# Kernel tuning notes

Measured on AMD Instinct MI355X. Metric: run time of the kernel, lower is better.

Reference implementation:

```python
import jax, jax.numpy as jnp
import numpy as np

B, S, D, H, L, DFF, WIN = 2, 2048, 768, 12, 2, 3072, 512
EPS = 1e-5
DH = D // H


def setup_inputs() -> dict:
    key = jax.random.key(0)
    ks = jax.random.split(key, 8)
    rn = lambda k, shape: jax.random.normal(k, shape, jnp.float32) * 0.02
    inp = {
        "src": jax.random.normal(ks[0], (B, S, D), jnp.float32),
        "qw": rn(ks[1], (L, D, D)), "qb": jnp.zeros((L, D), jnp.float32),
        "kw": rn(ks[2], (L, D, D)), "kb": jnp.zeros((L, D), jnp.float32),
        "vw": rn(ks[3], (L, D, D)), "vb": jnp.zeros((L, D), jnp.float32),
        "ow": rn(ks[4], (L, D, D)), "ob": jnp.zeros((L, D), jnp.float32),
        "w1": rn(ks[5], (L, DFF, D)), "b1": jnp.zeros((L, DFF), jnp.float32),
        "w2": rn(ks[6], (L, D, DFF)), "b2": jnp.zeros((L, D), jnp.float32),
        "g1": jnp.ones((L, D), jnp.float32), "be1": jnp.zeros((L, D), jnp.float32),
        "g2": jnp.ones((L, D), jnp.float32), "be2": jnp.zeros((L, D), jnp.float32),
    }
    return inp


def _ln(x, g, b):
    m = jnp.mean(x, axis=-1, keepdims=True)
    v = jnp.mean(jnp.square(x - m), axis=-1, keepdims=True)
    return (x - m) * jax.lax.rsqrt(v + EPS) * g + b


def _encoder(src, qw, qb, kw, kb, vw, vb, ow, ob, w1, b1, w2, b2, g1, be1, g2, be2):
    scale = DH ** -0.5
    idx = jnp.arange(S)
    # non-causal sliding window: |i - j| <= window_size // 2
    band = jnp.abs(idx[:, None] - idx[None, :]) <= (WIN // 2)
    neg = -jnp.finfo(jnp.float32).max
    x = src
    for l in range(L):
        # projections -> (B, H, S, DH)
        q = (x @ qw[l].T + qb[l]).reshape(B, S, H, DH).transpose(0, 2, 1, 3)
        k = (x @ kw[l].T + kb[l]).reshape(B, S, H, DH).transpose(0, 2, 1, 3)
        v = (x @ vw[l].T + vb[l]).reshape(B, S, H, DH).transpose(0, 2, 1, 3)
        # full dense scores then band mask (faithful to the original module)
        sim = jnp.einsum('bhid,bhjd->bhij', q * scale, k)
        sim = jnp.where(band, sim, neg)
        attn = jax.nn.softmax(sim, axis=-1)
        o = jnp.einsum('bhij,bhjd->bhid', attn, v)
        o = o.transpose(0, 2, 1, 3).reshape(B, S, D) @ ow[l].T + ob[l]
        # post-norm transformer block (norm_first=False)
        x = _ln(x + o, g1[l], be1[l])
        ff = jax.nn.relu(x @ w1[l].T + b1[l]) @ w2[l].T + b2[l]
        x = _ln(x + ff, g2[l], be2[l])
    return x


def reference(src, qw, qb, kw, kb, vw, vb, ow, ob, w1, b1, w2, b2, g1, be1, g2, be2):
    return _encoder(src, qw, qb, kw, kb, vw, vb, ow, ob, w1, b1, w2, b2, g1, be1, g2, be2)
```

## Files before the change

### kernel.cpp

```cpp
#include <hip/hip_runtime.h>
#include <math.h>

#define BATCH 2
#define SEQ   2048
#define DM    768
#define NHD   12
#define NL    2
#define DFF   3072
#define DH    64
#define HW    256
#define MR    (BATCH*SEQ)
#define EPSF  1e-5f
#define SCALE 0.125f
#define QKVS  2304

typedef __attribute__((ext_vector_type(8))) __bf16 bf16x8;
typedef __attribute__((ext_vector_type(4))) float  f32x4;

__device__ __forceinline__ ushort f2bu(float f) {
    union { __bf16 h; ushort u; } c;
    c.h = (__bf16)f;
    return c.u;
}
__device__ __forceinline__ float bu2f(ushort u) {
    union { uint u; float f; } c;
    c.u = ((uint)u) << 16;
    return c.f;
}

__device__ __forceinline__ void gload16(const ushort* g, ushort* l) {
    __builtin_amdgcn_global_load_lds(
        (const __attribute__((address_space(1))) void*)g,
        (__attribute__((address_space(3))) void*)l, 16, 0, 0);
}

__device__ __forceinline__ void xcd_swz(int& bx, int& by, int& bz) {
    const int gx = gridDim.x, gy = gridDim.y;
    const int nwg = gx * gy * gridDim.z;
    int lin = bx + gx * (by + gy * bz);
    lin = (lin & 7) * (nwg >> 3) + (lin >> 3);
    bx = lin % gx;
    int rest = lin / gx;
    by = rest % gy;
    bz = rest / gy;
}

__global__ __launch_bounds__(256) void cvt(const float* __restrict__ in,
                                           ushort* __restrict__ out, int n)
{
    int i = (blockIdx.x * 256 + threadIdx.x) * 4;
    if (i >= n) return;
    float4 v = *(const float4*)(in + i);
    ushort4 o;
    o.x = f2bu(v.x); o.y = f2bu(v.y); o.z = f2bu(v.z); o.w = f2bu(v.w);
    *(ushort4*)(out + i) = o;
}

#define STAGE128(bi, kt) do {                                           \
        const int _k0 = (kt) * 32;                                      \
        gload16(ag + _k0,                    &As[bi][t * 8]);           \
        gload16(ag + (size_t)64 * ldk + _k0, &As[bi][2048 + t * 8]);    \
        gload16(wg + _k0,                    &Ws[bi][t * 8]);           \
        gload16(wg + (size_t)64 * ldk + _k0, &Ws[bi][2048 + t * 8]);    \
    } while (0)

__global__ __launch_bounds__(256) void gemm128(
    const ushort* __restrict__ A, const ushort* __restrict__ W,
    const float* __restrict__ bias, ushort* __restrict__ C,
    float* __restrict__ part, int M, int N, int Kc, int ldk, int relu)
{
    __shared__ ushort As[3][128 * 32];
    __shared__ ushort Ws[3][128 * 32];

    int bxi = blockIdx.x, byi = blockIdx.y, bzi = blockIdx.z;
    xcd_swz(bxi, byi, bzi);

    const int t  = threadIdx.x;
    const int bm = byi * 128;
    const int bn = bxi * 128;
    const int z  = bzi;
    const int kbase = z * Kc;

    const int w    = t >> 6;
    const int lane = t & 63;
    const int quad = lane >> 4;
    const int lrow = lane & 15;
    const int wm   = (w >> 1) * 64;
    const int wn   = (w & 1) * 64;
    const int rx   = (lrow >> 1) & 3;
    const int rq   = (quad ^ rx) * 8;

    const int srow = t >> 2;
    const int scol = (((t & 3) ^ ((t >> 3) & 3)) * 8);
    const ushort* ag = A + (size_t)(bm + srow) * ldk + kbase + scol;
    const ushort* wg = W + (size_t)(bn + srow) * ldk + kbase + scol;

    f32x4 acc[4][4] = {};
    const int NT = Kc / 32;

    STAGE128(0, 0);
    STAGE128(1, 1);

    for (int kt = 0; kt < NT; ++kt) {
        if (kt + 1 < NT)
            asm volatile("s_waitcnt vmcnt(4)" ::: "memory");
        else
            asm volatile("s_waitcnt vmcnt(0)" ::: "memory");
        __builtin_amdgcn_s_barrier();

        const int cb = kt % 3;
        bf16x8 af[4], bfr[4];
#pragma unroll
        for (int i = 0; i < 4; ++i)
            af[i] = *(const bf16x8*)&As[cb][(wm + i * 16 + lrow) * 32 + rq];
#pragma unroll
        for (int j = 0; j < 4; ++j)
            bfr[j] = *(const bf16x8*)&Ws[cb][(wn + j * 16 + lrow) * 32 + rq];

#pragma unroll
        for (int i = 0; i < 4; ++i)
#pragma unroll
            for (int j = 0; j < 4; ++j)
                acc[i][j] = __builtin_amdgcn_mfma_f32_16x16x32_bf16(
                    af[i], bfr[j], acc[i][j], 0, 0, 0);

        if (kt + 2 < NT) {
            const int sb = (kt + 2) % 3;
            STAGE128(sb, kt + 2);
        }
    }

    if (gridDim.z > 1) {
        float* po = part + (size_t)z * M * N;
#pragma unroll
        for (int j = 0; j < 4; ++j) {
            const int col = bn + wn + j * 16 + lrow;
#pragma unroll
            for (int i = 0; i < 4; ++i) {
                const int rb = bm + wm + i * 16 + quad * 4;
#pragma unroll
                for (int r = 0; r < 4; ++r)
                    po[(size_t)(rb + r) * N + col] = acc[i][j][r];
            }
        }
    } else {
#pragma unroll
        for (int j = 0; j < 4; ++j) {
            const int col = bn + wn + j * 16 + lrow;
            const float bv = bias[col];
#pragma unroll
            for (int i = 0; i < 4; ++i) {
                const int rb = bm + wm + i * 16 + quad * 4;
#pragma unroll
                for (int r = 0; r < 4; ++r) {
                    float vv = acc[i][j][r] + bv;
                    if (relu) vv = fmaxf(vv, 0.f);
                    C[(size_t)(rb + r) * N + col] = f2bu(vv);
                }
            }
        }
    }
}

#define STAGE64(bi, kt) do {                                            \
        const int _k0 = (kt) * 32;                                      \
        gload16(ag + _k0,                    &As[bi][t * 8]);           \
        gload16(wg + _k0,                    &Ws[bi][t * 8]);           \
        gload16(wg + (size_t)64 * ldk + _k0, &Ws[bi][2048 + t * 8]);    \
    } while (0)

__global__ __launch_bounds__(256) void gemm64(
    const ushort* __restrict__ A, const ushort* __restrict__ W,
    const float* __restrict__ bias, ushort* __restrict__ C,
    float* __restrict__ part, int M, int N, int Kc, int ldk, int relu)
{
    __shared__ ushort As[3][64 * 32];
    __shared__ ushort Ws[3][128 * 32];

    int bxi = blockIdx.x, byi = blockIdx.y, bzi = blockIdx.z;
    xcd_swz(bxi, byi, bzi);

    const int t  = threadIdx.x;
    const int bm = byi * 64;
    const int bn = bxi * 128;
    const int z  = bzi;
    const int kbase = z * Kc;

    const int w    = t >> 6;
    const int lane = t & 63;
    const int quad = lane >> 4;
    const int lrow = lane & 15;
    const int wm   = (w >> 1) * 32;
    const int wn   = (w & 1) * 64;
    const int rx   = (lrow >> 1) & 3;
    const int rq   = (quad ^ rx) * 8;

    const int srow = t >> 2;
    const int scol = (((t & 3) ^ ((t >> 3) & 3)) * 8);
    const ushort* ag = A + (size_t)(bm + srow) * ldk + kbase + scol;
    const ushort* wg = W + (size_t)(bn + srow) * ldk + kbase + scol;

    f32x4 acc[2][4] = {};
    const int NT = Kc / 32;

    STAGE64(0, 0);
    STAGE64(1, 1);

    for (int kt = 0; kt < NT; ++kt) {
        if (kt + 1 < NT)
            asm volatile("s_waitcnt vmcnt(3)" ::: "memory");
        else
            asm volatile("s_waitcnt vmcnt(0)" ::: "memory");
        __builtin_amdgcn_s_barrier();

        const int cb = kt % 3;
        bf16x8 af[2], bfr[4];
#pragma unroll
        for (int i = 0; i < 2; ++i)
            af[i] = *(const bf16x8*)&As[cb][(wm + i * 16 + lrow) * 32 + rq];
#pragma unroll
        for (int j = 0; j < 4; ++j)
            bfr[j] = *(const bf16x8*)&Ws[cb][(wn + j * 16 + lrow) * 32 + rq];

#pragma unroll
        for (int i = 0; i < 2; ++i)
#pragma unroll
            for (int j = 0; j < 4; ++j)
                acc[i][j] = __builtin_amdgcn_mfma_f32_16x16x32_bf16(
                    af[i], bfr[j], acc[i][j], 0, 0, 0);

        if (kt + 2 < NT) {
            const int sb = (kt + 2) % 3;
            STAGE64(sb, kt + 2);
        }
    }

    if (gridDim.z > 1) {
        float* po = part + (size_t)z * M * N;
#pragma unroll
        for (int j = 0; j < 4; ++j) {
            const int col = bn + wn + j * 16 + lrow;
#pragma unroll
            for (int i = 0; i < 2; ++i) {
                const int rb = bm + wm + i * 16 + quad * 4;
#pragma unroll
                for (int r = 0; r < 4; ++r)
                    po[(size_t)(rb + r) * N + col] = acc[i][j][r];
            }
        }
    } else {
#pragma unroll
        for (int j = 0; j < 4; ++j) {
            const int col = bn + wn + j * 16 + lrow;
            const float bv = bias[col];
#pragma unroll
            for (int i = 0; i < 2; ++i) {
                const int rb = bm + wm + i * 16 + quad * 4;
#pragma unroll
                for (int r = 0; r < 4; ++r) {
                    float vv = acc[i][j][r] + bv;
                    if (relu) vv = fmaxf(vv, 0.f);
                    C[(size_t)(rb + r) * N + col] = f2bu(vv);
                }
            }
        }
    }
}

#define QT  64
#define NCH 9
#define KP  72

__global__ __launch_bounds__(256) void attn(
    const ushort* __restrict__ q, const ushort* __restrict__ k,
    const ushort* __restrict__ v, ushort* __restrict__ o)
{
    __shared__ ushort kv[2][64][KP];
    __shared__ ushort vt[2][64][KP];
    __shared__ ushort sc[QT][KP];

    int bxi = blockIdx.x, byi = blockIdx.y, bzi = blockIdx.z;
    xcd_swz(bxi, byi, bzi);

    const int t    = threadIdx.x;
    const int i0   = bxi * QT;
    const int h    = byi;
    const int b    = bzi;
    const size_t ibase = (size_t)b * SEQ * QKVS + (size_t)h * DH;
    const size_t obase = (size_t)b * SEQ * DM   + (size_t)h * DH;

    const int w    = t >> 6;
    const int lane = t & 63;
    const int quad = lane >> 4;
    const int lrow = lane & 15;
    const int qrow = w * 16;

    const int jstart = i0 - HW;

    const int sjj[2] = { t >> 3, (t + 256) >> 3 };
    const int sd0 = (t & 7) * 8;

#pragma unroll
    for (int e = 0; e < 2; ++e) {
        int idx = t + 256 * e;
        int qi = idx >> 3, d0 = (idx & 7) * 8;
        uint4 raw = *(const uint4*)(q + ibase + (size_t)(i0 + qi) * QKVS + d0);
        *(uint4*)&sc[qi][d0] = raw;
    }
    uint4 kr[2], vr[2];
#pragma unroll
    for (int e = 0; e < 2; ++e) {
        int j = jstart + sjj[e];
        kr[e] = make_uint4(0, 0, 0, 0);
        vr[e] = make_uint4(0, 0, 0, 0);
        if (j >= 0 && j < SEQ) {
            kr[e] = *(const uint4*)(k + ibase + (size_t)j * QKVS + sd0);
            vr[e] = *(const uint4*)(v + ibase + (size_t)j * QKVS + sd0);
        }
    }
#pragma unroll
    for (int e = 0; e < 2; ++e) {
        *(uint4*)&kv[0][sjj[e]][sd0] = kr[e];
        const ushort* u = (const ushort*)&vr[e];
#pragma unroll
        for (int x = 0; x < 8; ++x) {
            int dh  = sd0 + x;
            int blk = ((sjj[e] >> 3) ^ (dh >> 3)) & 7;
            vt[0][dh][blk * 8 + (sjj[e] & 7)] = u[x];
        }
    }
    __syncthreads();

    const bf16x8 a0 = *(const bf16x8*)&sc[qrow + lrow][quad * 8];
    const bf16x8 a1 = *(const bf16x8*)&sc[qrow + lrow][32 + quad * 8];

    float m_s = -1e20f, l_s = 0.f;
    f32x4 oacc[4] = {};

    for (int c = 0; c < NCH; ++c) {
        const int cur = c & 1;
        const int j0  = jstart + c * 64;

        if (c + 1 < NCH) {
            const int j0n = jstart + (c + 1) * 64;
#pragma unroll
            for (int e = 0; e < 2; ++e) {
                int j = j0n + sjj[e];
                kr[e] = make_uint4(0, 0, 0, 0);
                vr[e] = make_uint4(0, 0, 0, 0);
                if (j >= 0 && j < SEQ) {
                    kr[e] = *(const uint4*)(k + ibase + (size_t)j * QKVS + sd0);
                    vr[e] = *(const uint4*)(v + ibase + (size_t)j * QKVS + sd0);
                }
            }
        }

        const bool full = (c >= 1) && (c <= 7) && (j0 >= 0) && (j0 + 64 <= SEQ);
        float p[4][4];
#pragma unroll
        for (int kt = 0; kt < 4; ++kt) {
            const int krow = kt * 16;
            bf16x8 kf0 = *(const bf16x8*)&kv[cur][krow + lrow][quad * 8];
            bf16x8 kf1 = *(const bf16x8*)&kv[cur][krow + lrow][32 + quad * 8];
            f32x4 acc = {};
            acc = __builtin_amdgcn_mfma_f32_16x16x32_bf16(kf0, a0, acc, 0, 0, 0);
            acc = __builtin_amdgcn_mfma_f32_16x16x32_bf16(kf1, a1, acc, 0, 0, 0);
            if (full) {
#pragma unroll
                for (int r = 0; r < 4; ++r) p[kt][r] = acc[r] * SCALE;
            } else {
                const int ig = i0 + qrow + lrow;
#pragma unroll
                for (int r = 0; r < 4; ++r) {
                    const int jg = j0 + krow + quad * 4 + r;
                    bool ok = (jg >= 0) && (jg < SEQ) &&
                              (jg >= ig - HW) && (jg <= ig + HW);
                    p[kt][r] = ok ? acc[r] * SCALE : -1e30f;
                }
            }
        }

        float cm = p[0][0];
#pragma unroll
        for (int kt = 0; kt < 4; ++kt)
#pragma unroll
            for (int r = 0; r < 4; ++r) cm = fmaxf(cm, p[kt][r]);
        cm = fmaxf(cm, __shfl_xor(cm, 16));
        cm = fmaxf(cm, __shfl_xor(cm, 32));

        const bool resc = !__all(cm <= m_s + 8.f);
        float f = 1.f;
        if (resc) {
            const float mn = fmaxf(m_s, cm);
            f = __expf(m_s - mn);
            m_s = mn;
        }
        float cs = 0.f;
#pragma unroll
        for (int kt = 0; kt < 4; ++kt)
#pragma unroll
            for (int r = 0; r < 4; ++r) {
                float e = __expf(p[kt][r] - m_s);
                p[kt][r] = e;
                cs += e;
            }
        cs += __shfl_xor(cs, 16);
        cs += __shfl_xor(cs, 32);
        l_s = l_s * f + cs;
        if (resc) {
            float f4[4];
#pragma unroll
            for (int r = 0; r < 4; ++r) f4[r] = __shfl(f, quad * 4 + r);
#pragma unroll
            for (int nt = 0; nt < 4; ++nt)
#pragma unroll
                for (int r = 0; r < 4; ++r) oacc[nt][r] *= f4[r];
        }

#pragma unroll
        for (int kt = 0; kt < 4; ++kt) {
            ushort4 pw;
            pw.x = f2bu(p[kt][0]);
            pw.y = f2bu(p[kt][1]);
            pw.z = f2bu(p[kt][2]);
            pw.w = f2bu(p[kt][3]);
            *(ushort4*)&sc[qrow + lrow][kt * 16 + quad * 4] = pw;
        }

        bf16x8 pa0 = *(const bf16x8*)&sc[qrow + lrow][quad * 8];
        bf16x8 pa1 = *(const bf16x8*)&sc[qrow + lrow][32 + quad * 8];
#pragma unroll
        for (int nt = 0; nt < 4; ++nt) {
            const int dh  = nt * 16 + lrow;
            const int rsw = (dh >> 3) & 7;
            bf16x8 b0 = *(const bf16x8*)&vt[cur][dh][((quad)     ^ rsw) * 8];
            bf16x8 b1 = *(const bf16x8*)&vt[cur][dh][((quad + 4) ^ rsw) * 8];
            oacc[nt] = __builtin_amdgcn_mfma_f32_16x16x32_bf16(pa0, b0, oacc[nt], 0, 0, 0);
            oacc[nt] = __builtin_amdgcn_mfma_f32_16x16x32_bf16(pa1, b1, oacc[nt], 0, 0, 0);
        }

        if (c + 1 < NCH) {
            const int nxt = cur ^ 1;
#pragma unroll
            for (int e = 0; e < 2; ++e) {
                *(uint4*)&kv[nxt][sjj[e]][sd0] = kr[e];
                const ushort* u = (const ushort*)&vr[e];
#pragma unroll
                for (int x = 0; x < 8; ++x) {
                    int dh  = sd0 + x;
                    int blk = ((sjj[e] >> 3) ^ (dh >> 3)) & 7;
                    vt[nxt][dh][blk * 8 + (sjj[e] & 7)] = u[x];
                }
            }
        }
        __syncthreads();
    }

    const float inv = 1.f / l_s;
    float inv4[4];
#pragma unroll
    for (int r = 0; r < 4; ++r) inv4[r] = __shfl(inv, quad * 4 + r);
#pragma unroll
    for (int r = 0; r < 4; ++r) {
        const int qi = i0 + qrow + quad * 4 + r;
#pragma unroll
        for (int nt = 0; nt < 4; ++nt)
            o[obase + (size_t)qi * DM + nt * 16 + lrow] = f2bu(oacc[nt][r] * inv4[r]);
    }
}

__global__ __launch_bounds__(256) void add_ln_sk(
    const ushort* __restrict__ xa, const float* __restrict__ pp,
    const float* __restrict__ bias, const float* __restrict__ g,
    const float* __restrict__ be,
    ushort* __restrict__ ob, float* __restrict__ of, int fin)
{
    const int r = blockIdx.x * 4 + (threadIdx.x >> 6);
    const int t = threadIdx.x & 63;
    const size_t off = (size_t)r * DM;
    const size_t pl  = (size_t)MR * DM;
    float sv[12];
    float s1 = 0.f, s2 = 0.f;
#pragma unroll
    for (int ii = 0; ii < 12; ++ii) {
        const int c = t + 64 * ii;
        float vv = bu2f(xa[off + c]) + pp[off + c] + pp[pl + off + c] + bias[c];
        sv[ii] = vv; s1 += vv; s2 += vv * vv;
    }
#pragma unroll
    for (int o2 = 32; o2; o2 >>= 1) {
        s1 += __shfl_xor(s1, o2);
        s2 += __shfl_xor(s2, o2);
    }
    const float mean = s1 * (1.f / 768.f);
    const float rstd = rsqrtf(s2 * (1.f / 768.f) - mean * mean + EPSF);
#pragma unroll
    for (int ii = 0; ii < 12; ++ii) {
        const int c = t + 64 * ii;
        float v = (sv[ii] - mean) * rstd * g[c] + be[c];
        if (fin) of[off + c] = v;
        else     ob[off + c] = f2bu(v);
    }
}

__global__ __launch_bounds__(256) void add_ln_sk3(
    const ushort* __restrict__ xa, const float* __restrict__ pp,
    const float* __restrict__ bias, const float* __restrict__ g,
    const float* __restrict__ be,
    ushort* __restrict__ ob, float* __restrict__ of, int fin)
{
    const int r = blockIdx.x * 4 + (threadIdx.x >> 6);
    const int t = threadIdx.x & 63;
    const size_t off = (size_t)r * DM;
    const size_t pl  = (size_t)MR * DM;
    float sv[12];
    float s1 = 0.f, s2 = 0.f;
#pragma unroll
    for (int ii = 0; ii < 12; ++ii) {
        const int c = t + 64 * ii;
        float vv = bu2f(xa[off + c]) + pp[off + c] + pp[pl + off + c]
                 + pp[2 * pl + off + c] + bias[c];
        sv[ii] = vv; s1 += vv; s2 += vv * vv;
    }
#pragma unroll
    for (int o2 = 32; o2; o2 >>= 1) {
        s1 += __shfl_xor(s1, o2);
        s2 += __shfl_xor(s2, o2);
    }
    const float mean = s1 * (1.f / 768.f);
    const float rstd = rsqrtf(s2 * (1.f / 768.f) - mean * mean + EPSF);
#pragma unroll
    for (int ii = 0; ii < 12; ++ii) {
        const int c = t + 64 * ii;
        float v = (sv[ii] - mean) * rstd * g[c] + be[c];
        if (fin) of[off + c] = v;
        else     ob[off + c] = f2bu(v);
    }
}

extern "C" void kernel_launch(void* const* d_in, const int* in_sizes, int n_in,
                              void* d_out, int out_size, void* d_ws, size_t ws_size,
                              hipStream_t stream) {
    (void)in_sizes; (void)n_in; (void)out_size; (void)ws_size;
    const float* src = (const float*)d_in[0];
    const float* qw  = (const float*)d_in[1];
    const float* qb  = (const float*)d_in[2];
    const float* kw  = (const float*)d_in[3];
    const float* kb  = (const float*)d_in[4];
    const float* vw  = (const float*)d_in[5];
    const float* vb  = (const float*)d_in[6];
    const float* ow  = (const float*)d_in[7];
    const float* ob  = (const float*)d_in[8];
    const float* w1  = (const float*)d_in[9];
    const float* b1  = (const float*)d_in[10];
    const float* w2  = (const float*)d_in[11];
    const float* b2  = (const float*)d_in[12];
    const float* g1  = (const float*)d_in[13];
    const float* be1 = (const float*)d_in[14];
    const float* g2  = (const float*)d_in[15];
    const float* be2 = (const float*)d_in[16];

    const size_t A    = (size_t)MR * DM;
    const size_t WD1  = (size_t)DM * DM;
    const size_t WQKV = (size_t)3 * DM * DM;
    const size_t WF1  = (size_t)DFF * DM;
    const size_t WF   = (size_t)NL * WF1;

    float*  bcat = (float*)d_ws;
    ushort* p    = (ushort*)(bcat + (size_t)NL * QKVS);
    ushort* qkvwB = p; p += (size_t)NL * WQKV;
    ushort* owB   = p; p += (size_t)NL * WD1;
    ushort* w1B   = p; p += WF;
    ushort* w2B   = p; p += WF;
    ushort* xb    = p; p += A;
    ushort* qkvB  = p; p += 3 * A;
    ushort* oB    = p; p += A;
    ushort* yB    = p; p += A;
    ushort* h1    = p; p += A;
    ushort* ffh   = p; p += 4 * A;
    ushort* x2    = p;

    float* partF = (float*)xb;
    float* partO = (float*)ffh;

    for (int l = 0; l < NL; ++l) {
        hipMemcpyAsync(bcat + (size_t)l * QKVS + 0,    qb + (size_t)l * DM,
                       DM * sizeof(float), hipMemcpyDeviceToDevice, stream);
        hipMemcpyAsync(bcat + (size_t)l * QKVS + DM,   kb + (size_t)l * DM,
                       DM * sizeof(float), hipMemcpyDeviceToDevice, stream);
        hipMemcpyAsync(bcat + (size_t)l * QKVS + 2*DM, vb + (size_t)l * DM,
                       DM * sizeof(float), hipMemcpyDeviceToDevice, stream);
    }

    for (int l = 0; l < NL; ++l) {
        cvt<<<(int)(WD1 / 1024), 256, 0, stream>>>(
            qw + (size_t)l * WD1, qkvwB + (size_t)l * WQKV + 0,     (int)WD1);
        cvt<<<(int)(WD1 / 1024), 256, 0, stream>>>(
            kw + (size_t)l * WD1, qkvwB + (size_t)l * WQKV + WD1,   (int)WD1);
        cvt<<<(int)(WD1 / 1024), 256, 0, stream>>>(
            vw + (size_t)l * WD1, qkvwB + (size_t)l * WQKV + 2*WD1, (int)WD1);
    }
    cvt<<<(int)(NL * WD1 / 1024), 256, 0, stream>>>(ow, owB, (int)(NL * WD1));
    cvt<<<(int)(WF / 1024), 256, 0, stream>>>(w1, w1B, (int)WF);
    cvt<<<(int)(WF / 1024), 256, 0, stream>>>(w2, w2B, (int)WF);
    cvt<<<(int)(A  / 1024), 256, 0, stream>>>(src, xb, (int)A);

    const dim3 gQKV(QKVS / 128, MR / 128);
    const dim3 gOp(DM / 128, MR / 64, 2);
    const dim3 gF1(DFF / 128, MR / 128);
    const dim3 gF2(DM / 128, MR / 128, 3);
    const dim3 gA(SEQ / QT, NHD, BATCH);

    for (int l = 0; l < NL; ++l) {
        const size_t bD = (size_t)l * DM;
        const size_t bF = (size_t)l * DFF;
        const ushort* xin = (l == 0) ? xb : x2;

        gemm128<<<gQKV, 256, 0, stream>>>(xin, qkvwB + (size_t)l * WQKV,
                                          bcat + (size_t)l * QKVS, qkvB,
                                          nullptr, MR, QKVS, DM, DM, 0);
        attn<<<gA, 256, 0, stream>>>(qkvB, qkvB + DM, qkvB + 2 * DM, oB);
        gemm64<<<gOp, 256, 0, stream>>>(oB, owB + (size_t)l * WD1, nullptr,
                                        nullptr, partO, MR, DM, DM / 2, DM, 0);
        add_ln_sk<<<MR / 4, 256, 0, stream>>>(xin, partO, ob + bD,
                                              g1 + bD, be1 + bD,
                                              h1, nullptr, 0);
        gemm128<<<gF1, 256, 0, stream>>>(h1, w1B + (size_t)l * WF1, b1 + bF, ffh,
                                         nullptr, MR, DFF, DM, DM, 1);
        gemm128<<<gF2, 256, 0, stream>>>(ffh, w2B + (size_t)l * WF1, nullptr,
                                         nullptr, partF, MR, DM, DFF / 3, DFF, 0);
        if (l == NL - 1)
            add_ln_sk3<<<MR / 4, 256, 0, stream>>>(h1, partF, b2 + bD,
                                                   g2 + bD, be2 + bD,
                                                   nullptr, (float*)d_out, 1);
        else
            add_ln_sk3<<<MR / 4, 256, 0, stream>>>(h1, partF, b2 + bD,
                                                   g2 + bD, be2 + bD,
                                                   x2, nullptr, 0);
    }
}
```

Measured before the change: 455.5 us.

## Batch bias/weight conversion launches and raise wave priority around MFMA blocks

Replaces six device-to-device memcpys with a single bias-concatenation kernel, and six per-layer QKV weight conversion launches with a single 2D-grid cvt3 kernel. This cuts launch and copy overhead in the per-call preprocessing. Separately, it wraps the MFMA loops in the GEMM and attention kernels with s_setprio raises so waves issuing matrix ops get scheduling priority over waves doing loads. The priority hints may help or hurt interleaving, depending on occupancy.

```diff
diff --git a/kernel.cpp b/kernel.cpp
--- a/kernel.cpp
+++ b/kernel.cpp
@@ -56,6 +56,41 @@
     *(ushort4*)(out + i) = o;
 }
 
+__global__ __launch_bounds__(256) void cvt3(
+    const float* __restrict__ s0, const float* __restrict__ s1,
+    const float* __restrict__ s2, ushort* __restrict__ dst,
+    int seg, int dstride)
+{
+    const int l = blockIdx.y;
+    int i = (blockIdx.x * 256 + threadIdx.x) * 4;
+    if (i >= 3 * seg) return;
+    const float* s;
+    int off;
+    if (i < seg)           { s = s0 + (size_t)l * seg; off = i; }
+    else if (i < 2 * seg)  { s = s1 + (size_t)l * seg; off = i - seg; }
+    else                   { s = s2 + (size_t)l * seg; off = i - 2 * seg; }
+    float4 v = *(const float4*)(s + off);
+    ushort4 o;
+    o.x = f2bu(v.x); o.y = f2bu(v.y); o.z = f2bu(v.z); o.w = f2bu(v.w);
+    *(ushort4*)(dst + (size_t)l * dstride + i) = o;
+}
+
+__global__ __launch_bounds__(256) void bias_cat(
+    const float* __restrict__ qb, const float* __restrict__ kb,
+    const float* __restrict__ vb, float* __restrict__ bcat)
+{
+    const int b = blockIdx.x;
+    const int l = b / 3, wsel = b % 3;
+    const float* s = (wsel == 0) ? qb : (wsel == 1) ? kb : vb;
+    s += (size_t)l * DM;
+    float* d = bcat + (size_t)l * QKVS + wsel * DM;
+#pragma unroll
+    for (int e = 0; e < 3; ++e) {
+        int c = threadIdx.x + 256 * e;
+        d[c] = s[c];
+    }
+}
+
 #define STAGE128(bi, kt) do {                                           \
         const int _k0 = (kt) * 32;                                      \
         gload16(ag + _k0,                    &As[bi][t * 8]);           \
@@ -117,12 +152,14 @@
         for (int j = 0; j < 4; ++j)
             bfr[j] = *(const bf16x8*)&Ws[cb][(wn + j * 16 + lrow) * 32 + rq];
 
+        __builtin_amdgcn_s_setprio(1);
 #pragma unroll
         for (int i = 0; i < 4; ++i)
 #pragma unroll
             for (int j = 0; j < 4; ++j)
                 acc[i][j] = __builtin_amdgcn_mfma_f32_16x16x32_bf16(
                     af[i], bfr[j], acc[i][j], 0, 0, 0);
+        __builtin_amdgcn_s_setprio(0);
 
         if (kt + 2 < NT) {
             const int sb = (kt + 2) % 3;
@@ -222,12 +259,14 @@
         for (int j = 0; j < 4; ++j)
             bfr[j] = *(const bf16x8*)&Ws[cb][(wn + j * 16 + lrow) * 32 + rq];
 
+        __builtin_amdgcn_s_setprio(1);
 #pragma unroll
         for (int i = 0; i < 2; ++i)
 #pragma unroll
             for (int j = 0; j < 4; ++j)
                 acc[i][j] = __builtin_amdgcn_mfma_f32_16x16x32_bf16(
                     af[i], bfr[j], acc[i][j], 0, 0, 0);
+        __builtin_amdgcn_s_setprio(0);
 
         if (kt + 2 < NT) {
             const int sb = (kt + 2) % 3;
@@ -363,8 +402,10 @@
             bf16x8 kf0 = *(const bf16x8*)&kv[cur][krow + lrow][quad * 8];
             bf16x8 kf1 = *(const bf16x8*)&kv[cur][krow + lrow][32 + quad * 8];
             f32x4 acc = {};
+            __builtin_amdgcn_s_setprio(1);
             acc = __builtin_amdgcn_mfma_f32_16x16x32_bf16(kf0, a0, acc, 0, 0, 0);
             acc = __builtin_amdgcn_mfma_f32_16x16x32_bf16(kf1, a1, acc, 0, 0, 0);
+            __builtin_amdgcn_s_setprio(0);
             if (full) {
 #pragma unroll
                 for (int r = 0; r < 4; ++r) p[kt][r] = acc[r] * SCALE;
@@ -429,6 +470,7 @@
 
         bf16x8 pa0 = *(const bf16x8*)&sc[qrow + lrow][quad * 8];
         bf16x8 pa1 = *(const bf16x8*)&sc[qrow + lrow][32 + quad * 8];
+        __builtin_amdgcn_s_setprio(1);
 #pragma unroll
         for (int nt = 0; nt < 4; ++nt) {
             const int dh  = nt * 16 + lrow;
@@ -438,6 +480,7 @@
             oacc[nt] = __builtin_amdgcn_mfma_f32_16x16x32_bf16(pa0, b0, oacc[nt], 0, 0, 0);
             oacc[nt] = __builtin_amdgcn_mfma_f32_16x16x32_bf16(pa1, b1, oacc[nt], 0, 0, 0);
         }
+        __builtin_amdgcn_s_setprio(0);
 
         if (c + 1 < NCH) {
             const int nxt = cur ^ 1;
@@ -583,22 +626,10 @@
     float* partF = (float*)xb;
     float* partO = (float*)ffh;
 
-    for (int l = 0; l < NL; ++l) {
-        hipMemcpyAsync(bcat + (size_t)l * QKVS + 0,    qb + (size_t)l * DM,
-                       DM * sizeof(float), hipMemcpyDeviceToDevice, stream);
-        hipMemcpyAsync(bcat + (size_t)l * QKVS + DM,   kb + (size_t)l * DM,
-                       DM * sizeof(float), hipMemcpyDeviceToDevice, stream);
-        hipMemcpyAsync(bcat + (size_t)l * QKVS + 2*DM, vb + (size_t)l * DM,
-                       DM * sizeof(float), hipMemcpyDeviceToDevice, stream);
-    }
-
-    for (int l = 0; l < NL; ++l) {
-        cvt<<<(int)(WD1 / 1024), 256, 0, stream>>>(
-            qw + (size_t)l * WD1, qkvwB + (size_t)l * WQKV + 0,     (int)WD1);
-        cvt<<<(int)(WD1 / 1024), 256, 0, stream>>>(
-            kw + (size_t)l * WD1, qkvwB + (size_t)l * WQKV + WD1,   (int)WD1);
-        cvt<<<(int)(WD1 / 1024), 256, 0, stream>>>(
-            vw + (size_t)l * WD1, qkvwB + (size_t)l * WQKV + 2*WD1, (int)WD1);
+    bias_cat<<<NL * 3, 256, 0, stream>>>(qb, kb, vb, bcat);
+    {
+        dim3 g3((int)(3 * WD1 / 1024), NL);
+        cvt3<<<g3, 256, 0, stream>>>(qw, kw, vw, qkvwB, (int)WD1, (int)WQKV);
     }
     cvt<<<(int)(NL * WD1 / 1024), 256, 0, stream>>>(ow, owB, (int)(NL * WD1));
     cvt<<<(int)(WF / 1024), 256, 0, stream>>>(w1, w1B, (int)WF);
```

After: 432.0 us, median of 2. 1.05x faster.

## Fuse weight prep into one kernel, widen attention tiles, add MFMA priority hints

Applied to the files above, without the earlier changes.

Replaces the many per-tensor conversion launches and bias memcpys with a single prep kernel that converts all weights and the input to bf16 and gathers the QKV biases. The attention kernel now uses 128-query tiles with 512 threads and 10 key chunks, with per-wave full-chunk bounds, so more queries share each K/V chunk load. s_setprio hints are placed around the MFMA blocks in the GEMMs and attention to favour matrix work over memory issue. The changes cut launch overhead and K/V reload traffic, but larger attention blocks mean fewer workgroups (384 instead of 768) and more masked work per tile.

```diff
diff --git a/kernel.cpp b/kernel.cpp
--- a/kernel.cpp
+++ b/kernel.cpp
@@ -45,15 +45,87 @@
     bz = rest / gy;
 }
 
-__global__ __launch_bounds__(256) void cvt(const float* __restrict__ in,
-                                           ushort* __restrict__ out, int n)
+__global__ __launch_bounds__(256) void prep(
+    const float* __restrict__ qw, const float* __restrict__ kw,
+    const float* __restrict__ vw, const float* __restrict__ ow,
+    const float* __restrict__ w1, const float* __restrict__ w2,
+    const float* __restrict__ src,
+    const float* __restrict__ qb, const float* __restrict__ kb,
+    const float* __restrict__ vb,
+    ushort* __restrict__ qkvwB, ushort* __restrict__ owB,
+    ushort* __restrict__ w1B, ushort* __restrict__ w2B,
+    ushort* __restrict__ xb, float* __restrict__ bcat)
 {
-    int i = (blockIdx.x * 256 + threadIdx.x) * 4;
-    if (i >= n) return;
-    float4 v = *(const float4*)(in + i);
-    ushort4 o;
-    o.x = f2bu(v.x); o.y = f2bu(v.y); o.z = f2bu(v.z); o.w = f2bu(v.w);
-    *(ushort4*)(out + i) = o;
+    const int WD1C  = DM * DM;
+    const int WQKVC = 3 * WD1C;
+    const int WF1C  = DFF * DM;
+    const int NB0 = NL * WQKVC / 1024;
+    const int NB1 = NL * WD1C / 1024;
+    const int NB2 = NL * WF1C / 1024;
+    const int NB4 = MR * DM / 1024;
+
+    int b = blockIdx.x;
+    const int tid = threadIdx.x;
+
+    if (b < NB0) {
+        int e = b * 1024 + tid * 4;
+        int l = e / WQKVC;
+        int r = e % WQKVC;
+        const float* s; int off;
+        if (r < WD1C)          { s = qw + (size_t)l * WD1C; off = r; }
+        else if (r < 2 * WD1C) { s = kw + (size_t)l * WD1C; off = r - WD1C; }
+        else                   { s = vw + (size_t)l * WD1C; off = r - 2 * WD1C; }
+        float4 v = *(const float4*)(s + off);
+        ushort4 o4;
+        o4.x = f2bu(v.x); o4.y = f2bu(v.y); o4.z = f2bu(v.z); o4.w = f2bu(v.w);
+        *(ushort4*)(qkvwB + (size_t)l * WQKVC + r) = o4;
+        return;
+    }
+    b -= NB0;
+    if (b < NB1) {
+        int i = b * 1024 + tid * 4;
+        float4 v = *(const float4*)(ow + i);
+        ushort4 o4;
+        o4.x = f2bu(v.x); o4.y = f2bu(v.y); o4.z = f2bu(v.z); o4.w = f2bu(v.w);
+        *(ushort4*)(owB + i) = o4;
+        return;
+    }
+    b -= NB1;
+    if (b < NB2) {
+        int i = b * 1024 + tid * 4;
+        float4 v = *(const float4*)(w1 + i);
+        ushort4 o4;
+        o4.x = f2bu(v.x); o4.y = f2bu(v.y); o4.z = f2bu(v.z); o4.w = f2bu(v.w);
+        *(ushort4*)(w1B + i) = o4;
+        return;
+    }
+    b -= NB2;
+    if (b < NB2) {
+        int i = b * 1024 + tid * 4;
+        float4 v = *(const float4*)(w2 + i);
+        ushort4 o4;
+        o4.x = f2bu(v.x); o4.y = f2bu(v.y); o4.z = f2bu(v.z); o4.w = f2bu(v.w);
+        *(ushort4*)(w2B + i) = o4;
+        return;
+    }
+    b -= NB2;
+    if (b < NB4) {
+        int i = b * 1024 + tid * 4;
+        float4 v = *(const float4*)(src + i);
+        ushort4 o4;
+        o4.x = f2bu(v.x); o4.y = f2bu(v.y); o4.z = f2bu(v.z); o4.w = f2bu(v.w);
+        *(ushort4*)(xb + i) = o4;
+        return;
+    }
+#pragma unroll
+    for (int e = 0; e < 18; ++e) {
+        int j = tid + 256 * e;
+        int l = j / (3 * DM);
+        int r = j % (3 * DM);
+        int sel = r / DM, off = r % DM;
+        const float* s = (sel == 0) ? qb : (sel == 1) ? kb : vb;
+        bcat[(size_t)l * QKVS + sel * DM + off] = s[(size_t)l * DM + off];
+    }
 }
 
 #define STAGE128(bi, kt) do {                                           \
@@ -117,12 +189,14 @@
         for (int j = 0; j < 4; ++j)
             bfr[j] = *(const bf16x8*)&Ws[cb][(wn + j * 16 + lrow) * 32 + rq];
 
+        __builtin_amdgcn_s_setprio(1);
 #pragma unroll
         for (int i = 0; i < 4; ++i)
 #pragma unroll
             for (int j = 0; j < 4; ++j)
                 acc[i][j] = __builtin_amdgcn_mfma_f32_16x16x32_bf16(
                     af[i], bfr[j], acc[i][j], 0, 0, 0);
+        __builtin_amdgcn_s_setprio(0);
 
         if (kt + 2 < NT) {
             const int sb = (kt + 2) % 3;
@@ -222,12 +296,14 @@
         for (int j = 0; j < 4; ++j)
             bfr[j] = *(const bf16x8*)&Ws[cb][(wn + j * 16 + lrow) * 32 + rq];
 
+        __builtin_amdgcn_s_setprio(1);
 #pragma unroll
         for (int i = 0; i < 2; ++i)
 #pragma unroll
             for (int j = 0; j < 4; ++j)
                 acc[i][j] = __builtin_amdgcn_mfma_f32_16x16x32_bf16(
                     af[i], bfr[j], acc[i][j], 0, 0, 0);
+        __builtin_amdgcn_s_setprio(0);
 
         if (kt + 2 < NT) {
             const int sb = (kt + 2) % 3;
@@ -267,11 +343,11 @@
     }
 }
 
-#define QT  64
-#define NCH 9
+#define QT  128
+#define NCH 10
 #define KP  72
 
-__global__ __launch_bounds__(256) void attn(
+__global__ __launch_bounds__(512) void attn(
     const ushort* __restrict__ q, const ushort* __restrict__ k,
     const ushort* __restrict__ v, ushort* __restrict__ o)
 {
@@ -296,37 +372,37 @@
     const int qrow = w * 16;
 
     const int jstart = i0 - HW;
-
-    const int sjj[2] = { t >> 3, (t + 256) >> 3 };
+    const int clo = (qrow + 78) >> 6;
+    const int chi = (qrow + 449) >> 6;
+
+    const int sjj = t >> 3;
     const int sd0 = (t & 7) * 8;
 
 #pragma unroll
     for (int e = 0; e < 2; ++e) {
-        int idx = t + 256 * e;
+        int idx = t + 512 * e;
         int qi = idx >> 3, d0 = (idx & 7) * 8;
         uint4 raw = *(const uint4*)(q + ibase + (size_t)(i0 + qi) * QKVS + d0);
         *(uint4*)&sc[qi][d0] = raw;
     }
-    uint4 kr[2], vr[2];
-#pragma unroll
-    for (int e = 0; e < 2; ++e) {
-        int j = jstart + sjj[e];
-        kr[e] = make_uint4(0, 0, 0, 0);
-        vr[e] = make_uint4(0, 0, 0, 0);
+    uint4 kr, vr;
+    {
+        int j = jstart + sjj;
+        kr = make_uint4(0, 0, 0, 0);
+        vr = make_uint4(0, 0, 0, 0);
         if (j >= 0 && j < SEQ) {
-            kr[e] = *(const uint4*)(k + ibase + (size_t)j * QKVS + sd0);
-            vr[e] = *(const uint4*)(v + ibase + (size_t)j * QKVS + sd0);
-        }
-    }
-#pragma unroll
-    for (int e = 0; e < 2; ++e) {
-        *(uint4*)&kv[0][sjj[e]][sd0] = kr[e];
-        const ushort* u = (const ushort*)&vr[e];
+            kr = *(const uint4*)(k + ibase + (size_t)j * QKVS + sd0);
+            vr = *(const uint4*)(v + ibase + (size_t)j * QKVS + sd0);
+        }
+    }
+    *(uint4*)&kv[0][sjj][sd0] = kr;
+    {
+        const ushort* u = (const ushort*)&vr;
 #pragma unroll
         for (int x = 0; x < 8; ++x) {
             int dh  = sd0 + x;
-            int blk = ((sjj[e] >> 3) ^ (dh >> 3)) & 7;
-            vt[0][dh][blk * 8 + (sjj[e] & 7)] = u[x];
+            int blk = ((sjj >> 3) ^ (dh >> 3)) & 7;
+            vt[0][dh][blk * 8 + (sjj & 7)] = u[x];
         }
     }
     __syncthreads();
@@ -342,20 +418,17 @@
         const int j0  = jstart + c * 64;
 
         if (c + 1 < NCH) {
-            const int j0n = jstart + (c + 1) * 64;
-#pragma unroll
-            for (int e = 0; e < 2; ++e) {
-                int j = j0n + sjj[e];
-                kr[e] = make_uint4(0, 0, 0, 0);
-                vr[e] = make_uint4(0, 0, 0, 0);
-                if (j >= 0 && j < SEQ) {
-                    kr[e] = *(const uint4*)(k + ibase + (size_t)j * QKVS + sd0);
-                    vr[e] = *(const uint4*)(v + ibase + (size_t)j * QKVS + sd0);
-                }
-            }
-        }
-
-        const bool full = (c >= 1) && (c <= 7) && (j0 >= 0) && (j0 + 64 <= SEQ);
+            int j = jstart + (c + 1) * 64 + sjj;
+            kr = make_uint4(0, 0, 0, 0);
+            vr = make_uint4(0, 0, 0, 0);
+            if (j >= 0 && j < SEQ) {
+                kr = *(const uint4*)(k + ibase + (size_t)j * QKVS + sd0);
+                vr = *(const uint4*)(v + ibase + (size_t)j * QKVS + sd0);
+            }
+        }
+
+        const bool full = (c >= clo) && (c <= chi) &&
+                          (j0 >= 0) && (j0 + 64 <= SEQ);
         float p[4][4];
 #pragma unroll
         for (int kt = 0; kt < 4; ++kt) {
@@ -363,8 +436,10 @@
             bf16x8 kf0 = *(const bf16x8*)&kv[cur][krow + lrow][quad * 8];
             bf16x8 kf1 = *(const bf16x8*)&kv[cur][krow + lrow][32 + quad * 8];
             f32x4 acc = {};
+            __builtin_amdgcn_s_setprio(1);
             acc = __builtin_amdgcn_mfma_f32_16x16x32_bf16(kf0, a0, acc, 0, 0, 0);
             acc = __builtin_amdgcn_mfma_f32_16x16x32_bf16(kf1, a1, acc, 0, 0, 0);
+            __builtin_amdgcn_s_setprio(0);
             if (full) {
 #pragma unroll
                 for (int r = 0; r < 4; ++r) p[kt][r] = acc[r] * SCALE;
@@ -429,6 +504,7 @@
 
         bf16x8 pa0 = *(const bf16x8*)&sc[qrow + lrow][quad * 8];
         bf16x8 pa1 = *(const bf16x8*)&sc[qrow + lrow][32 + quad * 8];
+        __builtin_amdgcn_s_setprio(1);
 #pragma unroll
         for (int nt = 0; nt < 4; ++nt) {
             const int dh  = nt * 16 + lrow;
@@ -438,19 +514,17 @@
             oacc[nt] = __builtin_amdgcn_mfma_f32_16x16x32_bf16(pa0, b0, oacc[nt], 0, 0, 0);
             oacc[nt] = __builtin_amdgcn_mfma_f32_16x16x32_bf16(pa1, b1, oacc[nt], 0, 0, 0);
         }
+        __builtin_amdgcn_s_setprio(0);
 
         if (c + 1 < NCH) {
             const int nxt = cur ^ 1;
-#pragma unroll
-            for (int e = 0; e < 2; ++e) {
-                *(uint4*)&kv[nxt][sjj[e]][sd0] = kr[e];
-                const ushort* u = (const ushort*)&vr[e];
-#pragma unroll
-                for (int x = 0; x < 8; ++x) {
-                    int dh  = sd0 + x;
-                    int blk = ((sjj[e] >> 3) ^ (dh >> 3)) & 7;
-                    vt[nxt][dh][blk * 8 + (sjj[e] & 7)] = u[x];
-                }
+            *(uint4*)&kv[nxt][sjj][sd0] = kr;
+            const ushort* u = (const ushort*)&vr;
+#pragma unroll
+            for (int x = 0; x < 8; ++x) {
+                int dh  = sd0 + x;
+                int blk = ((sjj >> 3) ^ (dh >> 3)) & 7;
+                vt[nxt][dh][blk * 8 + (sjj & 7)] = u[x];
             }
         }
         __syncthreads();
@@ -583,27 +657,10 @@
     float* partF = (float*)xb;
     float* partO = (float*)ffh;
 
-    for (int l = 0; l < NL; ++l) {
-        hipMemcpyAsync(bcat + (size_t)l * QKVS + 0,    qb + (size_t)l * DM,
-                       DM * sizeof(float), hipMemcpyDeviceToDevice, stream);
-        hipMemcpyAsync(bcat + (size_t)l * QKVS + DM,   kb + (size_t)l * DM,
-                       DM * sizeof(float), hipMemcpyDeviceToDevice, stream);
-        hipMemcpyAsync(bcat + (size_t)l * QKVS + 2*DM, vb + (size_t)l * DM,
-                       DM * sizeof(float), hipMemcpyDeviceToDevice, stream);
-    }
-
-    for (int l = 0; l < NL; ++l) {
-        cvt<<<(int)(WD1 / 1024), 256, 0, stream>>>(
-            qw + (size_t)l * WD1, qkvwB + (size_t)l * WQKV + 0,     (int)WD1);
-        cvt<<<(int)(WD1 / 1024), 256, 0, stream>>>(
-            kw + (size_t)l * WD1, qkvwB + (size_t)l * WQKV + WD1,   (int)WD1);
-        cvt<<<(int)(WD1 / 1024), 256, 0, stream>>>(
-            vw + (size_t)l * WD1, qkvwB + (size_t)l * WQKV + 2*WD1, (int)WD1);
-    }
-    cvt<<<(int)(NL * WD1 / 1024), 256, 0, stream>>>(ow, owB, (int)(NL * WD1));
-    cvt<<<(int)(WF / 1024), 256, 0, stream>>>(w1, w1B, (int)WF);
-    cvt<<<(int)(WF / 1024), 256, 0, stream>>>(w2, w2B, (int)WF);
-    cvt<<<(int)(A  / 1024), 256, 0, stream>>>(src, xb, (int)A);
+    const int PB = (int)((NL * WQKV + NL * WD1 + 2 * WF + A) / 1024) + 1;
+    prep<<<PB, 256, 0, stream>>>(qw, kw, vw, ow, w1, w2, src,
+                                 qb, kb, vb,
+                                 qkvwB, owB, w1B, w2B, xb, bcat);
 
     const dim3 gQKV(QKVS / 128, MR / 128);
     const dim3 gOp(DM / 128, MR / 64, 2);
@@ -619,7 +676,7 @@
         gemm128<<<gQKV, 256, 0, stream>>>(xin, qkvwB + (size_t)l * WQKV,
                                           bcat + (size_t)l * QKVS, qkvB,
                                           nullptr, MR, QKVS, DM, DM, 0);
-        attn<<<gA, 256, 0, stream>>>(qkvB, qkvB + DM, qkvB + 2 * DM, oB);
+        attn<<<gA, 512, 0, stream>>>(qkvB, qkvB + DM, qkvB + 2 * DM, oB);
         gemm64<<<gOp, 256, 0, stream>>>(oB, owB + (size_t)l * WD1, nullptr,
                                         nullptr, partO, MR, DM, DM / 2, DM, 0);
         add_ln_sk<<<MR / 4, 256, 0, stream>>>(xin, partO, ob + bD,
```

New measurement: 432.3 us. 1.05x faster.
